# Performance work log

Measured on AMD Instinct MI355X. Metric: run time of the kernel, lower is better.

## Reference

```python
import jax, jax.numpy as jnp
import numpy as np

D_MODEL = 1024
NUM_HEADS = 16
D_K = D_MODEL // NUM_HEADS
B, S = 4, 2048


def setup_inputs() -> dict:
    key = jax.random.key(0)
    ks = jax.random.split(key, 9)
    scale = 1.0 / np.sqrt(D_MODEL)
    x = jax.random.normal(ks[0], (B, S, D_MODEL), dtype=jnp.float32)
    Wq = jax.random.uniform(ks[1], (D_MODEL, D_MODEL), jnp.float32, -scale, scale)
    bq = jax.random.uniform(ks[2], (D_MODEL,), jnp.float32, -scale, scale)
    Wk = jax.random.uniform(ks[3], (D_MODEL, D_MODEL), jnp.float32, -scale, scale)
    bk = jax.random.uniform(ks[4], (D_MODEL,), jnp.float32, -scale, scale)
    Wv = jax.random.uniform(ks[5], (D_MODEL, D_MODEL), jnp.float32, -scale, scale)
    bv = jax.random.uniform(ks[6], (D_MODEL,), jnp.float32, -scale, scale)
    Wo = jax.random.uniform(ks[7], (D_MODEL, D_MODEL), jnp.float32, -scale, scale)
    bo = jax.random.uniform(ks[8], (D_MODEL,), jnp.float32, -scale, scale)
    return {"x": x, "Wq": Wq, "bq": bq, "Wk": Wk, "bk": bk,
            "Wv": Wv, "bv": bv, "Wo": Wo, "bo": bo}


def reference(x, Wq, bq, Wk, bk, Wv, bv, Wo, bo):
    Bsz, Sl, _ = x.shape
    # Linear: x @ W.T + b (torch nn.Linear convention), then split heads -> (B,H,S,d_k)
    def proj(W, b):
        h = jnp.einsum('bsd,ed->bse', x, W) + b
        return h.reshape(Bsz, Sl, NUM_HEADS, D_K).transpose(0, 2, 1, 3)
    q = proj(Wq, bq)
    k = proj(Wk, bk)
    v = proj(Wv, bv)
    scores = jnp.einsum('bhqd,bhkd->bhqk', q, k) / np.sqrt(D_K)
    causal = jnp.tril(jnp.ones((Sl, Sl), dtype=bool))  # True = keep
    scores = jnp.where(causal[None, None], scores, -jnp.inf)
    attn = jax.nn.softmax(scores, axis=-1)
    out = jnp.einsum('bhqk,bhkd->bhqd', attn, v)
    out = out.transpose(0, 2, 1, 3).reshape(Bsz, Sl, D_MODEL)
    return jnp.einsum('bsd,ed->bse', out, Wo) + bo
```

## Files before the change

kernel.cpp:

```cpp
#include <hip/hip_runtime.h>
#include <hip/hip_bf16.h>

typedef __attribute__((ext_vector_type(8))) short short8;
typedef __attribute__((ext_vector_type(4))) short short4v;
typedef __attribute__((ext_vector_type(4))) float floatx4;
typedef unsigned short u16;

#define B_SZ 4
#define NH   16
#define SEQ  2048
#define DM   1024
#define DK   64
#define M_ROWS (B_SZ * SEQ)

__device__ __forceinline__ u16 f2bf(float f) {
  unsigned u = __float_as_uint(f);
  u += 0x7fff + ((u >> 16) & 1);
  return (u16)(u >> 16);
}

__device__ __forceinline__ void async_copy16(const u16* g, const short* lds) {
  __builtin_amdgcn_global_load_lds(
      (const __attribute__((address_space(1))) void*)g,
      (__attribute__((address_space(3))) void*)lds,
      16, 0, 0);
}

__global__ __launch_bounds__(256)
void cvt_kernel(const float* __restrict__ in, u16* __restrict__ out, int n4)
{
  for (int i = blockIdx.x * 256 + threadIdx.x; i < n4; i += gridDim.x * 256) {
    floatx4 v = ((const floatx4*)in)[i];
    short4v s;
#pragma unroll
    for (int e = 0; e < 4; ++e) s[e] = (short)f2bf(v[e]);
    ((short4v*)out)[i] = s;
  }
}

__device__ __forceinline__ void gemm_core_async(
    const u16* __restrict__ A, const float* __restrict__ W,
    int m0, int n0, floatx4 acc[4][4])
{
  __shared__ short As[128 * 32];
  __shared__ short Bs[128 * 40];

  const int tid  = threadIdx.x;
  const int w    = tid >> 6;
  const int lane = tid & 63;
  const int wm   = w >> 1, wn = w & 1;
  const int quad = lane >> 4, l16 = lane & 15;
  const int r4   = lane >> 2, c4 = lane & 3;

#pragma unroll
  for (int i = 0; i < 4; ++i)
#pragma unroll
    for (int j = 0; j < 4; ++j)
      acc[i][j] = floatx4{0.f, 0.f, 0.f, 0.f};

  for (int kt = 0; kt < (DM >> 5); ++kt) {
    const int kk = kt * 32;
    __syncthreads();
#pragma unroll
    for (int c = 0; c < 2; ++c) {
      const int rowA = w * 32 + c * 16;
      async_copy16(A + (size_t)(m0 + rowA + r4) * DM + kk + c4 * 8, As + rowA * 32);
    }
#pragma unroll
    for (int c = 0; c < 2; ++c) {
      const int idx = tid + c * 256;
      const int row = idx >> 2;
      const int col = (idx & 3) * 8;
      const float* pw = W + (size_t)(n0 + row) * DM + kk + col;
      floatx4 b0 = *(const floatx4*)pw, b1 = *(const floatx4*)(pw + 4);
      short8 sb;
#pragma unroll
      for (int e = 0; e < 4; ++e) { sb[e] = (short)f2bf(b0[e]); sb[4 + e] = (short)f2bf(b1[e]); }
      *(short8*)(Bs + row * 40 + col) = sb;
    }
    __syncthreads();

    short8 afr[4], bfr[4];
#pragma unroll
    for (int t = 0; t < 4; ++t) {
      afr[t] = *(const short8*)(As + (wm * 64 + t * 16 + l16) * 32 + quad * 8);
      bfr[t] = *(const short8*)(Bs + (wn * 64 + t * 16 + l16) * 40 + quad * 8);
    }
#pragma unroll
    for (int i = 0; i < 4; ++i)
#pragma unroll
      for (int j = 0; j < 4; ++j)
        acc[i][j] = __builtin_amdgcn_mfma_f32_16x16x32_bf16(afr[i], bfr[j], acc[i][j], 0, 0, 0);
  }
}

__global__ __launch_bounds__(256, 2)
void qkv_kernel(const u16* __restrict__ xb,
                const float* __restrict__ Wq, const float* __restrict__ Wk, const float* __restrict__ Wv,
                const float* __restrict__ bq, const float* __restrict__ bk, const float* __restrict__ bv,
                u16* __restrict__ Qo, u16* __restrict__ Ko, u16* __restrict__ Vto)
{
  const int mat = blockIdx.y >> 3;
  const int m0  = blockIdx.x * 128;
  const int n0  = (blockIdx.y & 7) * 128;
  const float* W    = (mat == 0) ? Wq : (mat == 1) ? Wk : Wv;
  const float* bias = (mat == 0) ? bq : (mat == 1) ? bk : bv;
  u16* dst          = (mat == 0) ? Qo : (mat == 1) ? Ko : Vto;

  floatx4 acc[4][4];
  gemm_core_async(xb, W, m0, n0, acc);

  const int tid = threadIdx.x;
  const int w = tid >> 6, lane = tid & 63;
  const int wm = w >> 1, wn = w & 1, quad = lane >> 4, l16 = lane & 15;

#pragma unroll
  for (int nt = 0; nt < 4; ++nt) {
    const int n = n0 + wn * 64 + nt * 16 + l16;
    const float bb = bias[n];
    const int h = n >> 6, d = n & 63;
#pragma unroll
    for (int mt = 0; mt < 4; ++mt)
#pragma unroll
      for (int r = 0; r < 4; ++r) {
        const int m = m0 + wm * 64 + mt * 16 + quad * 4 + r;
        const int b = m >> 11, s = m & 2047;
        const float v = acc[mt][nt][r] + bb;
        size_t off;
        if (mat < 2) off = ((size_t)(b * NH + h) * SEQ + s) * DK + d;
        else         off = ((size_t)(b * NH + h) * DK + d) * SEQ + s;
        dst[off] = f2bf(v);
      }
  }
}

#define AT_STR 72
__global__ __launch_bounds__(256, 2)
void attn_kernel(const u16* __restrict__ Q, const u16* __restrict__ Kx,
                 const u16* __restrict__ Vt, u16* __restrict__ O)
{
  __shared__ short Ks[64 * 64];
  __shared__ short Vs[64 * 64];
  __shared__ short Ps[4 * 32 * AT_STR];

  const int bh  = blockIdx.x;
  const int qtb = 15 - (int)blockIdx.y;
  const int q0  = qtb * 128;
  const int tid = threadIdx.x;
  const int w = tid >> 6, lane = tid & 63;
  const int quad = lane >> 4, l16 = lane & 15;
  const int r8 = lane >> 3, c8 = lane & 7;

  const u16* Qh = Q  + (size_t)bh * SEQ * DK;
  const u16* Kh = Kx + (size_t)bh * SEQ * DK;
  const u16* Vh = Vt + (size_t)bh * DK * SEQ;

  short8 qf[2][2];
#pragma unroll
  for (int qp = 0; qp < 2; ++qp) {
    const int qrow = q0 + w * 32 + qp * 16 + l16;
#pragma unroll
    for (int h = 0; h < 2; ++h)
      qf[qp][h] = *(const short8*)(Qh + (size_t)qrow * DK + h * 32 + quad * 8);
  }

  short8 vone;
#pragma unroll
  for (int j = 0; j < 8; ++j) vone[j] = (l16 == 0) ? (short)0x3F80 : (short)0;

  floatx4 o[2][4], ls[2];
#pragma unroll
  for (int qp = 0; qp < 2; ++qp) {
    ls[qp] = floatx4{0.f, 0.f, 0.f, 0.f};
#pragma unroll
    for (int dt = 0; dt < 4; ++dt) o[qp][dt] = floatx4{0.f, 0.f, 0.f, 0.f};
  }

  const float SC2 = 0.18033688011f;
  const int ktmax = 2 * qtb + 2;

  for (int kt = 0; kt < ktmax; ++kt) {
    const int k0 = kt * 64;
    __syncthreads();
#pragma unroll
    for (int c = 0; c < 2; ++c) {
      const int row8 = w * 16 + c * 8;
      const int sw   = (c8 ^ r8) * 8;
      async_copy16(Kh + (size_t)(k0 + row8 + r8) * DK + sw, Ks + row8 * 64);
      async_copy16(Vh + (size_t)(row8 + r8) * SEQ + k0 + sw, Vs + row8 * 64);
    }
    __syncthreads();

    short8 kf[4][2], vf[4][2];
#pragma unroll
    for (int nt = 0; nt < 4; ++nt)
#pragma unroll
      for (int h = 0; h < 2; ++h) {
        kf[nt][h] = *(const short8*)(Ks + (nt * 16 + l16) * 64 + (((h * 4 + quad) ^ (l16 & 7)) * 8));
        vf[nt][h] = *(const short8*)(Vs + (nt * 16 + l16) * 64 + (((h * 4 + quad) ^ (l16 & 7)) * 8));
      }

#pragma unroll
    for (int qp = 0; qp < 2; ++qp) {
      const int frag0 = q0 + w * 32 + qp * 16;
      if (k0 <= frag0 + 15) {
        floatx4 sc[4];
#pragma unroll
        for (int nt = 0; nt < 4; ++nt) {
          floatx4 z = floatx4{0.f, 0.f, 0.f, 0.f};
          z = __builtin_amdgcn_mfma_f32_16x16x32_bf16(qf[qp][0], kf[nt][0], z, 0, 0, 0);
          z = __builtin_amdgcn_mfma_f32_16x16x32_bf16(qf[qp][1], kf[nt][1], z, 0, 0, 0);
          sc[nt] = z;
        }
        const bool diag = (k0 + 63 > frag0);
#pragma unroll
        for (int nt = 0; nt < 4; ++nt)
#pragma unroll
          for (int r = 0; r < 4; ++r) {
            float s = sc[nt][r] * SC2;
            if (diag) {
              const int col = k0 + nt * 16 + l16;
              const int row = frag0 + quad * 4 + r;
              if (col > row) s = -1e30f;
            }
            sc[nt][r] = __builtin_amdgcn_exp2f(s);
          }
        short* Pp = Ps + (w * 32 + qp * 16) * AT_STR;
#pragma unroll
        for (int nt = 0; nt < 4; ++nt)
#pragma unroll
          for (int r = 0; r < 4; ++r)
            Pp[(quad * 4 + r) * AT_STR + nt * 16 + l16] = (short)f2bf(sc[nt][r]);
        short8 pf[2];
#pragma unroll
        for (int h = 0; h < 2; ++h)
          pf[h] = *(const short8*)(Pp + l16 * AT_STR + h * 32 + quad * 8);
#pragma unroll
        for (int dt = 0; dt < 4; ++dt) {
          o[qp][dt] = __builtin_amdgcn_mfma_f32_16x16x32_bf16(pf[0], vf[dt][0], o[qp][dt], 0, 0, 0);
          o[qp][dt] = __builtin_amdgcn_mfma_f32_16x16x32_bf16(pf[1], vf[dt][1], o[qp][dt], 0, 0, 0);
        }
        ls[qp] = __builtin_amdgcn_mfma_f32_16x16x32_bf16(pf[0], vone, ls[qp], 0, 0, 0);
        ls[qp] = __builtin_amdgcn_mfma_f32_16x16x32_bf16(pf[1], vone, ls[qp], 0, 0, 0);
      }
    }
  }

  const int b = bh >> 4, h = bh & 15;
#pragma unroll
  for (int qp = 0; qp < 2; ++qp) {
    const int frag0 = q0 + w * 32 + qp * 16;
#pragma unroll
    for (int r = 0; r < 4; ++r) {
      const float lv  = __shfl(ls[qp][r], lane & 48);
      const float inv = 1.0f / fmaxf(lv, 1e-20f);
      const int row   = frag0 + quad * 4 + r;
      const size_t base = ((size_t)b * SEQ + row) * DM + h * DK;
#pragma unroll
      for (int dt = 0; dt < 4; ++dt)
        O[base + dt * 16 + l16] = f2bf(o[qp][dt][r] * inv);
    }
  }
}

__global__ __launch_bounds__(256, 2)
void oproj_kernel(const u16* __restrict__ A, const float* __restrict__ Wo,
                  const float* __restrict__ bo, float* __restrict__ out)
{
  const int m0 = blockIdx.x * 128, n0 = blockIdx.y * 128;
  floatx4 acc[4][4];
  gemm_core_async(A, Wo, m0, n0, acc);

  const int tid = threadIdx.x;
  const int w = tid >> 6, lane = tid & 63;
  const int wm = w >> 1, wn = w & 1, quad = lane >> 4, l16 = lane & 15;

#pragma unroll
  for (int nt = 0; nt < 4; ++nt) {
    const int n = n0 + wn * 64 + nt * 16 + l16;
    const float bb = bo[n];
#pragma unroll
    for (int mt = 0; mt < 4; ++mt)
#pragma unroll
      for (int r = 0; r < 4; ++r) {
        const int m = m0 + wm * 64 + mt * 16 + quad * 4 + r;
        out[(size_t)m * DM + n] = acc[mt][nt][r] + bb;
      }
  }
}

extern "C" void kernel_launch(void* const* d_in, const int* in_sizes, int n_in,
                              void* d_out, int out_size, void* d_ws, size_t ws_size,
                              hipStream_t stream)
{
  const float* x  = (const float*)d_in[0];
  const float* Wq = (const float*)d_in[1];
  const float* bq = (const float*)d_in[2];
  const float* Wk = (const float*)d_in[3];
  const float* bk = (const float*)d_in[4];
  const float* Wv = (const float*)d_in[5];
  const float* bv = (const float*)d_in[6];
  const float* Wo = (const float*)d_in[7];
  const float* bo = (const float*)d_in[8];
  float* out = (float*)d_out;

  u16* qws  = (u16*)d_ws;
  u16* kws  = qws  + (size_t)M_ROWS * DM;
  u16* vtws = kws  + (size_t)M_ROWS * DM;
  u16* xb   = vtws + (size_t)M_ROWS * DM;
  u16* ows  = xb;

  cvt_kernel <<<dim3(2048), 256, 0, stream>>>(x, xb, (M_ROWS * DM) / 4);
  qkv_kernel <<<dim3(64, 24), 256, 0, stream>>>(xb, Wq, Wk, Wv, bq, bk, bv, qws, kws, vtws);
  attn_kernel<<<dim3(64, 16), 256, 0, stream>>>(qws, kws, vtws, ows);
  oproj_kernel<<<dim3(64, 8), 256, 0, stream>>>(ows, Wo, bo, out);
}
```

Baseline: 294.2 us.

## Pre-convert weights to bf16 and load both GEMM operands via async LDS copies

Wq/Wk/Wv are converted to bf16 together with x in one multi-matrix conversion kernel, and Wo in a separate small kernel just before the output projection. The GEMM core then loads both A and B tiles with global_load_lds async copies instead of converting fp32 weights to bf16 inside every tile iteration. This removes redundant per-block weight conversion and halves weight bytes read by the GEMMs. The cost is an extra launch and extra passes over the weights, plus scratch buffers reused from the output buffer and the Q workspace. The B tile loses its padding, which may add LDS bank conflicts.

```diff
diff --git a/kernel.cpp b/kernel.cpp
--- a/kernel.cpp
+++ b/kernel.cpp
@@ -27,7 +27,28 @@
 }
 
 __global__ __launch_bounds__(256)
-void cvt_kernel(const float* __restrict__ in, u16* __restrict__ out, int n4)
+void cvt4_kernel(const float* __restrict__ x,
+                 const float* __restrict__ wq, const float* __restrict__ wk,
+                 const float* __restrict__ wv,
+                 u16* __restrict__ xb, u16* __restrict__ wb)
+{
+  const int y = blockIdx.y;
+  const float* src; u16* dst; int n4;
+  if (y == 0)      { src = x;  dst = xb;                 n4 = (M_ROWS * DM) / 4; }
+  else if (y == 1) { src = wq; dst = wb;                 n4 = (DM * DM) / 4; }
+  else if (y == 2) { src = wk; dst = wb + DM * DM;       n4 = (DM * DM) / 4; }
+  else             { src = wv; dst = wb + 2 * DM * DM;   n4 = (DM * DM) / 4; }
+  for (int i = blockIdx.x * 256 + threadIdx.x; i < n4; i += gridDim.x * 256) {
+    floatx4 v = ((const floatx4*)src)[i];
+    short4v s;
+#pragma unroll
+    for (int e = 0; e < 4; ++e) s[e] = (short)f2bf(v[e]);
+    ((short4v*)dst)[i] = s;
+  }
+}
+
+__global__ __launch_bounds__(256)
+void cvt1_kernel(const float* __restrict__ in, u16* __restrict__ out, int n4)
 {
   for (int i = blockIdx.x * 256 + threadIdx.x; i < n4; i += gridDim.x * 256) {
     floatx4 v = ((const floatx4*)in)[i];
@@ -38,12 +59,12 @@
   }
 }
 
-__device__ __forceinline__ void gemm_core_async(
-    const u16* __restrict__ A, const float* __restrict__ W,
+__device__ __forceinline__ void gemm_core_bb(
+    const u16* __restrict__ A, const u16* __restrict__ Wb,
     int m0, int n0, floatx4 acc[4][4])
 {
   __shared__ short As[128 * 32];
-  __shared__ short Bs[128 * 40];
+  __shared__ short Bs[128 * 32];
 
   const int tid  = threadIdx.x;
   const int w    = tid >> 6;
@@ -64,19 +85,8 @@
 #pragma unroll
     for (int c = 0; c < 2; ++c) {
       const int rowA = w * 32 + c * 16;
-      async_copy16(A + (size_t)(m0 + rowA + r4) * DM + kk + c4 * 8, As + rowA * 32);
-    }
-#pragma unroll
-    for (int c = 0; c < 2; ++c) {
-      const int idx = tid + c * 256;
-      const int row = idx >> 2;
-      const int col = (idx & 3) * 8;
-      const float* pw = W + (size_t)(n0 + row) * DM + kk + col;
-      floatx4 b0 = *(const floatx4*)pw, b1 = *(const floatx4*)(pw + 4);
-      short8 sb;
-#pragma unroll
-      for (int e = 0; e < 4; ++e) { sb[e] = (short)f2bf(b0[e]); sb[4 + e] = (short)f2bf(b1[e]); }
-      *(short8*)(Bs + row * 40 + col) = sb;
+      async_copy16(A  + (size_t)(m0 + rowA + r4) * DM + kk + c4 * 8, As + rowA * 32);
+      async_copy16(Wb + (size_t)(n0 + rowA + r4) * DM + kk + c4 * 8, Bs + rowA * 32);
     }
     __syncthreads();
 
@@ -84,7 +94,7 @@
 #pragma unroll
     for (int t = 0; t < 4; ++t) {
       afr[t] = *(const short8*)(As + (wm * 64 + t * 16 + l16) * 32 + quad * 8);
-      bfr[t] = *(const short8*)(Bs + (wn * 64 + t * 16 + l16) * 40 + quad * 8);
+      bfr[t] = *(const short8*)(Bs + (wn * 64 + t * 16 + l16) * 32 + quad * 8);
     }
 #pragma unroll
     for (int i = 0; i < 4; ++i)
@@ -95,20 +105,20 @@
 }
 
 __global__ __launch_bounds__(256, 2)
-void qkv_kernel(const u16* __restrict__ xb,
-                const float* __restrict__ Wq, const float* __restrict__ Wk, const float* __restrict__ Wv,
-                const float* __restrict__ bq, const float* __restrict__ bk, const float* __restrict__ bv,
+void qkv_kernel(const u16* __restrict__ xb, const u16* __restrict__ wb,
+                const float* __restrict__ bq, const float* __restrict__ bk,
+                const float* __restrict__ bv,
                 u16* __restrict__ Qo, u16* __restrict__ Ko, u16* __restrict__ Vto)
 {
   const int mat = blockIdx.y >> 3;
   const int m0  = blockIdx.x * 128;
   const int n0  = (blockIdx.y & 7) * 128;
-  const float* W    = (mat == 0) ? Wq : (mat == 1) ? Wk : Wv;
+  const u16* W      = wb + (size_t)mat * DM * DM;
   const float* bias = (mat == 0) ? bq : (mat == 1) ? bk : bv;
   u16* dst          = (mat == 0) ? Qo : (mat == 1) ? Ko : Vto;
 
   floatx4 acc[4][4];
-  gemm_core_async(xb, W, m0, n0, acc);
+  gemm_core_bb(xb, W, m0, n0, acc);
 
   const int tid = threadIdx.x;
   const int w = tid >> 6, lane = tid & 63;
@@ -264,12 +274,12 @@
 }
 
 __global__ __launch_bounds__(256, 2)
-void oproj_kernel(const u16* __restrict__ A, const float* __restrict__ Wo,
+void oproj_kernel(const u16* __restrict__ A, const u16* __restrict__ Wob,
                   const float* __restrict__ bo, float* __restrict__ out)
 {
   const int m0 = blockIdx.x * 128, n0 = blockIdx.y * 128;
   floatx4 acc[4][4];
-  gemm_core_async(A, Wo, m0, n0, acc);
+  gemm_core_bb(A, Wob, m0, n0, acc);
 
   const int tid = threadIdx.x;
   const int w = tid >> 6, lane = tid & 63;
@@ -307,11 +317,15 @@
   u16* qws  = (u16*)d_ws;
   u16* kws  = qws  + (size_t)M_ROWS * DM;
   u16* vtws = kws  + (size_t)M_ROWS * DM;
-  u16* xb   = vtws + (size_t)M_ROWS * DM;
-  u16* ows  = xb;
-
-  cvt_kernel <<<dim3(2048), 256, 0, stream>>>(x, xb, (M_ROWS * DM) / 4);
-  qkv_kernel <<<dim3(64, 24), 256, 0, stream>>>(xb, Wq, Wk, Wv, bq, bk, bv, qws, kws, vtws);
+  u16* ows  = vtws + (size_t)M_ROWS * DM;
+
+  u16* xb = (u16*)d_out;
+  u16* wb = xb + (size_t)M_ROWS * DM;
+  u16* wo_b = qws;
+
+  cvt4_kernel<<<dim3(1024, 4), 256, 0, stream>>>(x, Wq, Wk, Wv, xb, wb);
+  qkv_kernel <<<dim3(64, 24), 256, 0, stream>>>(xb, wb, bq, bk, bv, qws, kws, vtws);
   attn_kernel<<<dim3(64, 16), 256, 0, stream>>>(qws, kws, vtws, ows);
-  oproj_kernel<<<dim3(64, 8), 256, 0, stream>>>(ows, Wo, bo, out);
-}
+  cvt1_kernel<<<dim3(1024), 256, 0, stream>>>(Wo, wo_b, (DM * DM) / 4);
+  oproj_kernel<<<dim3(64, 8), 256, 0, stream>>>(ows, wo_b, bo, out);
+}
```

Measured after the change: 275.5 us. -6.4%, faster.
